# Performance work log

Measured on AMD Instinct MI355X. Metric: run time of the kernel, lower is better.

The kernel has to match this reference:

```python
import jax, jax.numpy as jnp
import numpy as np

NE, NPROC, E, D = 50000, 25000, 200000, 128
L, T = 3, 4  # layers, edge types: 0:e->e, 1:e->p, 2:p->p, 3:p->e


def setup_inputs() -> dict:
    key = jax.random.key(0)
    ks = jax.random.split(key, 17)
    s = 1.0 / np.sqrt(D)
    return {
        'x_elem': jax.random.normal(ks[0], (NE, D), jnp.float32),
        'x_proc': jax.random.normal(ks[1], (NPROC, D), jnp.float32),
        'W_src': jax.random.normal(ks[2], (L, T, D, D), jnp.float32) * s,
        'W_dst': jax.random.normal(ks[3], (L, T, D, D), jnp.float32) * s,
        'att_src': jax.random.normal(ks[4], (L, T, D), jnp.float32) * s,
        'att_dst': jax.random.normal(ks[5], (L, T, D), jnp.float32) * s,
        'bias': jax.random.normal(ks[6], (L, T, D), jnp.float32) * 0.01,
        'lin_W': jax.random.normal(ks[7], (D, 2), jnp.float32) * s,
        'lin_b': jnp.zeros((2,), jnp.float32),
        'ee_src': jax.random.randint(ks[8], (E,), 0, NE),
        'ee_dst': jax.random.randint(ks[9], (E,), 0, NE),
        'ep_src': jax.random.randint(ks[10], (E,), 0, NE),
        'ep_dst': jax.random.randint(ks[11], (E,), 0, NPROC),
        'pp_src': jax.random.randint(ks[12], (E,), 0, NPROC),
        'pp_dst': jax.random.randint(ks[13], (E,), 0, NPROC),
        'pe_src': jax.random.randint(ks[14], (E,), 0, NPROC),
        'pe_dst': jax.random.randint(ks[15], (E,), 0, NE),
    }


def _gat(x_s, x_d, src, dst, n_dst, Ws, Wd, a_s, a_d, b):
    # one GATConv (heads=1, negative_slope=0 -> relu, no self loops)
    hs = x_s @ Ws                       # [Ns, D]
    hd = x_d @ Wd                       # [Nd, D]
    es = hs @ a_s                       # [Ns]
    ed = hd @ a_d                       # [Nd]
    logit = jax.nn.relu(es[src] + ed[dst])              # [E]
    m = jax.ops.segment_max(logit, dst, num_segments=n_dst)
    m = jnp.where(jnp.isfinite(m), m, 0.0)              # empty segments
    w = jnp.exp(logit - m[dst])
    denom = jax.ops.segment_sum(w, dst, num_segments=n_dst)
    alpha = w / jnp.maximum(denom[dst], 1e-16)          # edge softmax per dst
    out = jax.ops.segment_sum(alpha[:, None] * hs[src], dst, num_segments=n_dst)
    return out + b


def reference(x_elem, x_proc, W_src, W_dst, att_src, att_dst, bias, lin_W, lin_b,
              ee_src, ee_dst, ep_src, ep_dst, pp_src, pp_dst, pe_src, pe_dst):
    xe, xp = x_elem, x_proc
    for l in range(L):
        ee = _gat(xe, xe, ee_src, ee_dst, NE, W_src[l, 0], W_dst[l, 0], att_src[l, 0], att_dst[l, 0], bias[l, 0])
        ep = _gat(xe, xp, ep_src, ep_dst, NPROC, W_src[l, 1], W_dst[l, 1], att_src[l, 1], att_dst[l, 1], bias[l, 1])
        pp = _gat(xp, xp, pp_src, pp_dst, NPROC, W_src[l, 2], W_dst[l, 2], att_src[l, 2], att_dst[l, 2], bias[l, 2])
        pe = _gat(xp, xe, pe_src, pe_dst, NE, W_src[l, 3], W_dst[l, 3], att_src[l, 3], att_dst[l, 3], bias[l, 3])
        xe = ee + pe   # to_hetero aggr='sum' per destination node type
        xp = ep + pp
    x = jnp.concatenate([xe, xp], axis=0) @ lin_W + lin_b  # G_aggr
    return x.mean(axis=0)  # [2]
```

## Files before the change

### kernel.cpp

```cpp
#include <hip/hip_runtime.h>

#define NE_N 50000
#define NP_N 25000
#define E_N 200000
#define DIM 128
#define LOG2E 1.4426950408889634f
#define NREP 1024

#define NCHK 32
#define CHK_E (E_N / NCHK)
#define TBL 16384

typedef __attribute__((ext_vector_type(8))) short short8;
typedef __attribute__((ext_vector_type(4))) float f32x4;
typedef __attribute__((ext_vector_type(2))) float f32x2;

static __device__ __forceinline__ ushort f2bf(float f) {
  unsigned x = __float_as_uint(f);
  return (ushort)((x + 0x7fffu + ((x >> 16) & 1u)) >> 16);
}
static __device__ __forceinline__ float bf2f(ushort u) {
  return __uint_as_float(((unsigned)u) << 16);
}

static __device__ __forceinline__ void gload_lds16(const void* g, void* l) {
  __builtin_amdgcn_global_load_lds(
      (const __attribute__((address_space(1))) void*)g,
      (__attribute__((address_space(3))) void*)l, 16, 0, 0);
}

#define HIST_BLKS (4 * NCHK)
#define HS_TOT (HIST_BLKS + 12 + 3)
__global__ __launch_bounds__(512) void hist_setup_k(
    const float* __restrict__ W_src, const float* __restrict__ W_dst,
    const float* __restrict__ att_dst, ushort* __restrict__ WbT,
    float* __restrict__ vec, const int* __restrict__ d0,
    const int* __restrict__ d1, const int* __restrict__ d2,
    const int* __restrict__ d3, unsigned char* __restrict__ h0,
    unsigned char* __restrict__ h1, unsigned char* __restrict__ h2,
    unsigned char* __restrict__ h3, ushort* __restrict__ rk0,
    ushort* __restrict__ rk1, ushort* __restrict__ rk2,
    ushort* __restrict__ rk3) {
  __shared__ int keys[TBL];
  __shared__ int cnts[TBL];
  const int blk = blockIdx.x;
  const int tid = threadIdx.x;
  if (blk < HIST_BLKS) {
    const int ty = blk >> 5, c = blk & (NCHK - 1);
    const int NN = (ty == 0 || ty == 3) ? NE_N : NP_N;
    const int* dst = ty == 0 ? d0 : ty == 1 ? d1 : ty == 2 ? d2 : d3;
    unsigned char* h = ty == 0 ? h0 : ty == 1 ? h1 : ty == 2 ? h2 : h3;
    ushort* rk = ty == 0 ? rk0 : ty == 1 ? rk1 : ty == 2 ? rk2 : rk3;
    for (int i = tid; i < TBL; i += 512) { keys[i] = -1; cnts[i] = 0; }
    __syncthreads();
    const int base = c * CHK_E;
    for (int i = tid; i < CHK_E; i += 512) {
      const int e = base + i;
      const int d = dst[e];
      unsigned hsh = ((unsigned)d * 2654435761u) >> 18;
      hsh &= (TBL - 1);
      int lr;
      while (true) {
        int prev = atomicCAS(&keys[hsh], -1, d);
        if (prev == -1 || prev == d) { lr = atomicAdd(&cnts[hsh], 1); break; }
        hsh = (hsh + 1) & (TBL - 1);
      }
      rk[e] = (ushort)lr;
    }
    __syncthreads();
    for (int i = tid; i < TBL; i += 512) {
      int k = keys[i];
      if (k >= 0) h[(size_t)c * NN + k] = (unsigned char)cnts[i];
    }
  } else if (blk < HIST_BLKS + 12) {
    const int w = blk - HIST_BLKS;
    const float* src = W_src + (size_t)w * DIM * DIM;
    ushort* dstw = WbT + (size_t)w * DIM * DIM;
    for (int i = tid; i < DIM * DIM; i += 512) {
      int k = i >> 7, n = i & 127;
      dstw[n * DIM + k] = f2bf(src[i]);
    }
  } else {
    const int b = blk - HIST_BLKS - 12;
    const int lt = b * 4 + (tid >> 7);
    const int i = tid & 127;
    const float* Wd = W_dst + (size_t)lt * DIM * DIM;
    const float* ad = att_dst + lt * DIM;
    float s = 0.f;
#pragma unroll 8
    for (int j = 0; j < DIM; j++) s += Wd[i * DIM + j] * ad[j];
    vec[lt * DIM + i] = s;
  }
}

__global__ __launch_bounds__(256) void scanA_k(
    unsigned char* __restrict__ h0, unsigned char* __restrict__ h1,
    unsigned char* __restrict__ h2, unsigned char* __restrict__ h3,
    int* __restrict__ c0, int* __restrict__ c1, int* __restrict__ c2,
    int* __restrict__ c3, int* __restrict__ part) {
  int ty = blockIdx.y;
  unsigned char* h = ty == 0 ? h0 : ty == 1 ? h1 : ty == 2 ? h2 : h3;
  int* cnt = ty == 0 ? c0 : ty == 1 ? c1 : ty == 2 ? c2 : c3;
  int n = (ty == 0 || ty == 3) ? NE_N : NP_N;
  int nblk = (n + 1023) >> 10;
  if ((int)blockIdx.x >= nblk) return;
  int base = blockIdx.x * 1024 + threadIdx.x * 4;
  int s = 0;
  if (base < n) {
    int run0 = 0, run1 = 0, run2 = 0, run3 = 0;
#pragma unroll
    for (int c = 0; c < NCHK; c++) {
      unsigned* hp = (unsigned*)(h + (size_t)c * n + base);
      unsigned v = *hp;
      *hp = (unsigned)(run0 & 255) | ((unsigned)(run1 & 255) << 8) |
            ((unsigned)(run2 & 255) << 16) | ((unsigned)(run3 & 255) << 24);
      run0 += (int)(v & 255u);
      run1 += (int)((v >> 8) & 255u);
      run2 += (int)((v >> 16) & 255u);
      run3 += (int)((v >> 24) & 255u);
    }
    cnt[base + 0] = run0; cnt[base + 1] = run1;
    cnt[base + 2] = run2; cnt[base + 3] = run3;
    s = run0 + run1 + run2 + run3;
  }
  int lane = threadIdx.x & 63, wid = threadIdx.x >> 6;
#pragma unroll
  for (int off = 32; off > 0; off >>= 1) s += __shfl_xor(s, off, 64);
  __shared__ int ws4[4];
  if (lane == 0) ws4[wid] = s;
  __syncthreads();
  if (threadIdx.x == 0)
    part[ty * 64 + blockIdx.x] = ws4[0] + ws4[1] + ws4[2] + ws4[3];
}

__global__ __launch_bounds__(256) void scanBC_k(
    const int* __restrict__ c0, const int* __restrict__ c1,
    const int* __restrict__ c2, const int* __restrict__ c3,
    int* __restrict__ r0, int* __restrict__ r1, int* __restrict__ r2,
    int* __restrict__ r3, const int* __restrict__ part) {
  int ty = blockIdx.y;
  int bx = blockIdx.x;
  const int* cnt = ty == 0 ? c0 : ty == 1 ? c1 : ty == 2 ? c2 : c3;
  int* rp = ty == 0 ? r0 : ty == 1 ? r1 : ty == 2 ? r2 : r3;
  int n = (ty == 0 || ty == 3) ? NE_N : NP_N;
  int nblk = (n + 1023) >> 10;
  if (bx >= nblk) return;

  __shared__ int s_excl;
  if (threadIdx.x < 64) {
    int pl = threadIdx.x;
    int v = (pl < nblk) ? part[ty * 64 + pl] : 0;
    int sc = v;
#pragma unroll
    for (int off = 1; off < 64; off <<= 1) {
      int t = __shfl_up(sc, off, 64);
      if (pl >= off) sc += t;
    }
    if (pl == bx) s_excl = sc - v;
  }
  if (bx == 0 && threadIdx.x == 0) rp[n] = E_N;
  __syncthreads();

  int base = bx * 1024 + threadIdx.x * 4;
  int v[4];
#pragma unroll
  for (int j = 0; j < 4; j++) v[j] = (base + j < n) ? cnt[base + j] : 0;
  int s = v[0] + v[1] + v[2] + v[3];
  int lane = threadIdx.x & 63, wid = threadIdx.x >> 6;
  int sc = s;
#pragma unroll
  for (int off = 1; off < 64; off <<= 1) {
    int t = __shfl_up(sc, off, 64);
    if (lane >= off) sc += t;
  }
  __shared__ int ws4[4];
  if (lane == 63) ws4[wid] = sc;
  __syncthreads();
  int wbase = 0;
  for (int w = 0; w < wid; w++) wbase += ws4[w];
  int p = s_excl + wbase + sc - s;
#pragma unroll
  for (int j = 0; j < 4; j++) {
    if (base + j < n) rp[base + j] = p;
    p += v[j];
  }
}

#define EBLK ((NE_N + 255) / 256)
#define PBLK ((NP_N + 255) / 256)
#define GEMM_BLK (EBLK + PBLK)
#define FILL_PER_CHK 13
#define FILL_BLKS (4 * NCHK * FILL_PER_CHK)
#define HG2_TOT (GEMM_BLK + FILL_BLKS)

template <bool FP32>
static __device__ __forceinline__ void x_prefetch(
    const void* xb, int rowA, int quad, float4* xraw, short8* xvv) {
  if (FP32) {
    const float* xf32 = (const float*)xb + (size_t)rowA * DIM + quad * 8;
#pragma unroll
    for (int k0 = 0; k0 < 4; k0++) {
      xraw[2 * k0] = *(const float4*)(xf32 + k0 * 32);
      xraw[2 * k0 + 1] = *(const float4*)(xf32 + k0 * 32 + 4);
    }
  } else {
    const ushort* xb16 = (const ushort*)xb + (size_t)rowA * DIM + quad * 8;
#pragma unroll
    for (int k0 = 0; k0 < 4; k0++)
      xvv[k0] = *(const short8*)(xb16 + k0 * 32);
  }
}

template <bool FP32>
static __device__ __forceinline__ void strip_body(
    int row0, int N, int m, int quad, int lane, const short8* wlds,
    const float* dv0, const float* dv1, const float* a0, const float* a1,
    unsigned char* hs0, unsigned char* hs1, float* es0, float* es1,
    float* edA, float* edB, float4* xraw, short8* xvv) {
  float edp0 = 0.f, edp1 = 0.f;
#pragma unroll
  for (int k0 = 0; k0 < 4; k0++) {
    float xf[8];
    if (FP32) {
      float4 f0 = xraw[2 * k0], f1 = xraw[2 * k0 + 1];
      xf[0] = f0.x; xf[1] = f0.y; xf[2] = f0.z; xf[3] = f0.w;
      xf[4] = f1.x; xf[5] = f1.y; xf[6] = f1.z; xf[7] = f1.w;
      short8 xv;
#pragma unroll
      for (int j = 0; j < 8; j++) xv[j] = (short)f2bf(xf[j]);
      xvv[k0] = xv;
    } else {
#pragma unroll
      for (int j = 0; j < 8; j++) xf[j] = bf2f((ushort)xvv[k0][j]);
    }
    int off = k0 * 32 + quad * 8;
    float4 vA0 = *(const float4*)&dv0[off];
    float4 vA1 = *(const float4*)&dv0[off + 4];
    float4 vB0 = *(const float4*)&dv1[off];
    float4 vB1 = *(const float4*)&dv1[off + 4];
    edp0 += xf[0] * vA0.x + xf[1] * vA0.y + xf[2] * vA0.z + xf[3] * vA0.w +
            xf[4] * vA1.x + xf[5] * vA1.y + xf[6] * vA1.z + xf[7] * vA1.w;
    edp1 += xf[0] * vB0.x + xf[1] * vB0.y + xf[2] * vB0.z + xf[3] * vB0.w +
            xf[4] * vB1.x + xf[5] * vB1.y + xf[6] * vB1.z + xf[7] * vB1.w;
  }

  f32x4 acc0[8], acc1[8];
#pragma unroll
  for (int f = 0; f < 8; f++) {
    acc0[f] = (f32x4){0.f, 0.f, 0.f, 0.f};
    acc1[f] = (f32x4){0.f, 0.f, 0.f, 0.f};
  }
#pragma unroll
  for (int k0 = 0; k0 < 4; k0++) {
    const short8 xv = xvv[k0];
#pragma unroll
    for (int f = 0; f < 8; f++) {
      acc0[f] = __builtin_amdgcn_mfma_f32_16x16x32_bf16(
          wlds[(k0 * 8 + f) * 64 + lane], xv, acc0[f], 0, 0, 0);
      acc1[f] = __builtin_amdgcn_mfma_f32_16x16x32_bf16(
          wlds[2048 + (k0 * 8 + f) * 64 + lane], xv, acc1[f], 0, 0, 0);
    }
  }

  const int row = row0 + m;
  edp0 += __shfl_xor(edp0, 16, 64);
  edp0 += __shfl_xor(edp0, 32, 64);
  edp1 += __shfl_xor(edp1, 16, 64);
  edp1 += __shfl_xor(edp1, 32, 64);
  if (quad == 0 && row < N) {
    edA[row] = edp0 * LOG2E;
    edB[row] = edp1 * LOG2E;
  }

#pragma unroll
  for (int set = 0; set < 2; set++) {
    f32x4* acc = set ? acc1 : acc0;
    const float* as = set ? a1 : a0;
    float* es = set ? es1 : es0;
    unsigned char* hs = set ? hs1 : hs0;

    float esum = 0.f;
#pragma unroll
    for (int f = 0; f < 8; f++) {
      float4 av = *(const float4*)&as[f * 16 + quad * 4];
      esum += acc[f][0] * av.x + acc[f][1] * av.y + acc[f][2] * av.z +
              acc[f][3] * av.w;
    }
    esum += __shfl_xor(esum, 16, 64);
    esum += __shfl_xor(esum, 32, 64);
    if (quad == 0 && row < N) es[row] = esum * LOG2E;

    if (row < N) {
#pragma unroll
      for (int f = 0; f < 8; f++) {
        int w = __builtin_amdgcn_cvt_pk_fp8_f32(acc[f][0], acc[f][1], 0, false);
        w = __builtin_amdgcn_cvt_pk_fp8_f32(acc[f][2], acc[f][3], w, true);
        *(unsigned*)&hs[(size_t)row * DIM + f * 16 + quad * 4] = (unsigned)w;
      }
    }
  }
}

template <bool FP32>
static __device__ __forceinline__ void gemm_body(
    int blk, const void* __restrict__ xev, const void* __restrict__ xpv,
    const ushort* __restrict__ WbT, const float* __restrict__ att,
    const float* __restrict__ vec, int l, unsigned char* __restrict__ hsE0,
    unsigned char* __restrict__ hsE1, unsigned char* __restrict__ hsP3,
    unsigned char* __restrict__ hsP2, float* __restrict__ esE0,
    float* __restrict__ esE1, float* __restrict__ esP3,
    float* __restrict__ esP2, float* __restrict__ edEA,
    float* __restrict__ edEB, float* __restrict__ edPA,
    float* __restrict__ edPB) {
  const void* xb;
  const ushort *W0T, *W1T;
  const float *a0, *a1, *dv0, *dv1;
  unsigned char *hs0, *hs1;
  float *es0, *es1, *edA, *edB;
  int N, rbase;
  if (blk < EBLK) {
    xb = xev; N = NE_N; rbase = blk * 256;
    W0T = WbT + (size_t)(l * 4 + 0) * DIM * DIM;
    W1T = WbT + (size_t)(l * 4 + 1) * DIM * DIM;
    a0 = att + (l * 4 + 0) * DIM; a1 = att + (l * 4 + 1) * DIM;
    dv0 = vec + (l * 4 + 0) * DIM; dv1 = vec + (l * 4 + 3) * DIM;
    hs0 = hsE0; hs1 = hsE1; es0 = esE0; es1 = esE1;
    edA = edEA; edB = edEB;
  } else {
    blk -= EBLK; xb = xpv; N = NP_N; rbase = blk * 256;
    W0T = WbT + (size_t)(l * 4 + 3) * DIM * DIM;
    W1T = WbT + (size_t)(l * 4 + 2) * DIM * DIM;
    a0 = att + (l * 4 + 3) * DIM; a1 = att + (l * 4 + 2) * DIM;
    dv0 = vec + (l * 4 + 1) * DIM; dv1 = vec + (l * 4 + 2) * DIM;
    hs0 = hsP3; hs1 = hsP2; es0 = esP3; es1 = esP2;
    edA = edPA; edB = edPB;
  }

  const int wave = threadIdx.x >> 6;
  const int lane = threadIdx.x & 63;
  const int m = lane & 15, quad = lane >> 4;
  const int row0A = rbase + wave * 16;
  const int row0B = rbase + 128 + wave * 16;
  int rowLA = row0A + m; if (rowLA >= N) rowLA = N - 1;
  int rowLB = row0B + m; if (rowLB >= N) rowLB = N - 1;

  float4 xrawA[8]; short8 xvvA[4];
  x_prefetch<FP32>(xb, rowLA, quad, xrawA, xvvA);

  __shared__ short8 wlds[4096];
  {
    const int i15 = lane & 15, i4 = lane >> 4;
#pragma unroll
    for (int r = 0; r < 8; r++) {
      const int g = r * 8 + wave;
      const int set = g >> 5, k0 = (g >> 3) & 3, f = g & 7;
      const ushort* WT = set ? W1T : W0T;
      gload_lds16(WT + (size_t)(f * 16 + i15) * DIM + k0 * 32 + i4 * 8,
                  &wlds[g * 64]);
    }
  }
  __syncthreads();

  float4 xrawB[8]; short8 xvvB[4];
  if (!FP32) x_prefetch<FP32>(xb, rowLB, quad, xrawB, xvvB);

  if (row0A < N)
    strip_body<FP32>(row0A, N, m, quad, lane, wlds, dv0, dv1, a0, a1,
                     hs0, hs1, es0, es1, edA, edB, xrawA, xvvA);
  if (FP32) x_prefetch<FP32>(xb, rowLB, quad, xrawB, xvvB);
  if (row0B < N)
    strip_body<FP32>(row0B, N, m, quad, lane, wlds, dv0, dv1, a0, a1,
                     hs0, hs1, es0, es1, edA, edB, xrawB, xvvB);
}

__global__ __launch_bounds__(512, 4) void gemm_k(
    const ushort* __restrict__ xe, const ushort* __restrict__ xp,
    const ushort* __restrict__ WbT, const float* __restrict__ att,
    const float* __restrict__ vec, int l, unsigned char* __restrict__ hsE0,
    unsigned char* __restrict__ hsE1, unsigned char* __restrict__ hsP3,
    unsigned char* __restrict__ hsP2, float* __restrict__ esE0,
    float* __restrict__ esE1, float* __restrict__ esP3,
    float* __restrict__ esP2, float* __restrict__ edEA,
    float* __restrict__ edEB, float* __restrict__ edPA,
    float* __restrict__ edPB) {
  gemm_body<false>(blockIdx.x, xe, xp, WbT, att, vec, l, hsE0, hsE1, hsP3,
                   hsP2, esE0, esE1, esP3, esP2, edEA, edEB, edPA, edPB);
}

__global__ __launch_bounds__(512, 4) void fill_gemm0_k(
    const float* __restrict__ xe, const float* __restrict__ xp,
    const ushort* __restrict__ WbT, const float* __restrict__ att,
    const float* __restrict__ vec, unsigned char* __restrict__ hsE0,
    unsigned char* __restrict__ hsE1, unsigned char* __restrict__ hsP3,
    unsigned char* __restrict__ hsP2, float* __restrict__ esE0,
    float* __restrict__ esE1, float* __restrict__ esP3,
    float* __restrict__ esP2, float* __restrict__ edEA,
    float* __restrict__ edEB, float* __restrict__ edPA,
    float* __restrict__ edPB, const int* __restrict__ s0,
    const int* __restrict__ s1, const int* __restrict__ s2,
    const int* __restrict__ s3, const int* __restrict__ d0,
    const int* __restrict__ d1, const int* __restrict__ d2,
    const int* __restrict__ d3, const ushort* __restrict__ rk0,
    const ushort* __restrict__ rk1, const ushort* __restrict__ rk2,
    const ushort* __restrict__ rk3, const int* __restrict__ r0,
    const int* __restrict__ r1, const int* __restrict__ r2,
    const int* __restrict__ r3, const unsigned char* __restrict__ h0,
    const unsigned char* __restrict__ h1, const unsigned char* __restrict__ h2,
    const unsigned char* __restrict__ h3, ushort* __restrict__ o0,
    ushort* __restrict__ o1, ushort* __restrict__ o2,
    ushort* __restrict__ o3) {
  const int blk = blockIdx.x;
  if (blk < GEMM_BLK) {
    gemm_body<true>(blk, xe, xp, WbT, att, vec, 0, hsE0, hsE1, hsP3, hsP2,
                    esE0, esE1, esP3, esP2, edEA, edEB, edPA, edPB);
  } else {
    const int fb = blk - GEMM_BLK;
    const int x = fb & 7, q = fb >> 3;
    const int g = ((q & 15) << 3) | x;
    const int j = q >> 4;
    const int i = j * 512 + threadIdx.x;
    if (i >= CHK_E) return;
    const int ty = g >> 5, c = g & 31;
    const int e = c * CHK_E + i;
    const int NN = (ty == 0 || ty == 3) ? NE_N : NP_N;
    const int* src = ty == 0 ? s0 : ty == 1 ? s1 : ty == 2 ? s2 : s3;
    const int* dst = ty == 0 ? d0 : ty == 1 ? d1 : ty == 2 ? d2 : d3;
    const ushort* rk = ty == 0 ? rk0 : ty == 1 ? rk1 : ty == 2 ? rk2 : rk3;
    const int* rp = ty == 0 ? r0 : ty == 1 ? r1 : ty == 2 ? r2 : r3;
    const unsigned char* ho = ty == 0 ? h0 : ty == 1 ? h1 : ty == 2 ? h2 : h3;
    ushort* out = ty == 0 ? o0 : ty == 1 ? o1 : ty == 2 ? o2 : o3;
    const int dd = dst[e];
    out[rp[dd] + (int)ho[(size_t)c * NN + dd] + (int)rk[e]] =
        (ushort)src[e];
  }
}

__global__ __launch_bounds__(256) void gat_gather_all(
    const int* __restrict__ rp0, const ushort* __restrict__ ss0,
    const int* __restrict__ rp1, const ushort* __restrict__ ss1,
    const int* __restrict__ rp2, const ushort* __restrict__ ss2,
    const int* __restrict__ rp3, const ushort* __restrict__ ss3,
    const float* __restrict__ esE0, const unsigned char* __restrict__ hsE0,
    const float* __restrict__ esE1, const unsigned char* __restrict__ hsE1,
    const float* __restrict__ esP3, const unsigned char* __restrict__ hsP3,
    const float* __restrict__ esP2, const unsigned char* __restrict__ hsP2,
    const float* __restrict__ edEA, const float* __restrict__ edEB,
    const float* __restrict__ edPA, const float* __restrict__ edPB,
    const float* __restrict__ bias, int l, ushort* __restrict__ outxe,
    ushort* __restrict__ outxp, int to_csum, float* __restrict__ csum_rep) {
  __shared__ float2 trx[4][8][64];
  const int wid = (blockIdx.x * 256 + threadIdx.x) >> 6;
  const int lane = threadIdx.x & 63;
  const int wv = threadIdx.x >> 6;
  const int slot = lane >> 3, sub = lane & 7;
  const int half = slot >> 2;
  const int hslot = slot & 3;
  const bool active = wid < NE_N + NP_N;

  float v0 = 0.f, v1 = 0.f;
  const float *b0 = bias, *b1 = bias;
  ushort* outb = outxe;
  int node = 0;

  if (active) {
    const int *rpA, *rpB;
    const ushort *ssA, *ssB;
    const float *esA, *esB;
    const unsigned char *hsA, *hsB;
    const float *edA, *edB;
    if (wid < NE_N) {
      node = wid;
      rpA = rp0; ssA = ss0; esA = esE0; hsA = hsE0;
      rpB = rp3; ssB = ss3; esB = esP3; hsB = hsP3;
      edA = edEA; edB = edEB;
      b0 = bias + (l * 4 + 0) * DIM; b1 = bias + (l * 4 + 3) * DIM;
      outb = outxe;
    } else {
      node = wid - NE_N;
      rpA = rp1; ssA = ss1; esA = esE1; hsA = hsE1;
      rpB = rp2; ssB = ss2; esB = esP2; hsB = hsP2;
      edA = edPA; edB = edPB;
      b0 = bias + (l * 4 + 1) * DIM; b1 = bias + (l * 4 + 2) * DIM;
      outb = outxp;
    }

    const int* rp = half ? rpB : rpA;
    const ushort* ss = half ? ssB : ssA;
    const float* es = half ? esB : esA;
    const unsigned char* hs = half ? hsB : hsA;
    const float edv = half ? edB[node] : edA[node];
    const int beg = rp[node], end = rp[node + 1];

    f32x2 acc2[8];
#pragma unroll
    for (int j = 0; j < 8; j++) acc2[j] = (f32x2){0.f, 0.f};
    float sw = 0.f;

    for (int e = beg + hslot; e < end; e += 4) {
      int s = ss[e];
      float w = exp2f(fmaxf(es[s] + edv, 0.f));
      sw += w;
      f32x2 w2 = {w, w};
      uint4 h = *(const uint4*)&hs[(size_t)s * DIM + sub * 16];
      acc2[0] += w2 * __builtin_amdgcn_cvt_pk_f32_fp8((int)h.x, false);
      acc2[1] += w2 * __builtin_amdgcn_cvt_pk_f32_fp8((int)h.x, true);
      acc2[2] += w2 * __builtin_amdgcn_cvt_pk_f32_fp8((int)h.y, false);
      acc2[3] += w2 * __builtin_amdgcn_cvt_pk_f32_fp8((int)h.y, true);
      acc2[4] += w2 * __builtin_amdgcn_cvt_pk_f32_fp8((int)h.z, false);
      acc2[5] += w2 * __builtin_amdgcn_cvt_pk_f32_fp8((int)h.z, true);
      acc2[6] += w2 * __builtin_amdgcn_cvt_pk_f32_fp8((int)h.w, false);
      acc2[7] += w2 * __builtin_amdgcn_cvt_pk_f32_fp8((int)h.w, true);
    }

    sw += __shfl_xor(sw, 8, 64);
    sw += __shfl_xor(sw, 16, 64);
    const float inv = 1.f / fmaxf(sw, 1e-16f);

#pragma unroll
    for (int j = 0; j < 8; j++)
      trx[wv][slot][(sub * 8 + j) ^ slot] =
          make_float2(acc2[j].x * inv, acc2[j].y * inv);
    float2 vv = trx[wv][0][(sub * 8 + slot) ^ 0];
#pragma unroll
    for (int s2 = 1; s2 < 8; s2++) {
      float2 t = trx[wv][s2][(sub * 8 + slot) ^ s2];
      vv.x += t.x;
      vv.y += t.y;
    }
    v0 = vv.x;
    v1 = vv.y;
  }

  const int d = sub * 16 + slot * 2;
  if (to_csum) {
    __shared__ float lsum[4][DIM];
    lsum[wv][d] = v0;
    lsum[wv][d + 1] = v1;
    __syncthreads();
    if (threadIdx.x < DIM) {
      float s = lsum[0][threadIdx.x] + lsum[1][threadIdx.x] +
                lsum[2][threadIdx.x] + lsum[3][threadIdx.x];
      float* rep = csum_rep + (size_t)(blockIdx.x & (NREP - 1)) * DIM;
      unsafeAtomicAdd(&rep[threadIdx.x], s);
    }
  } else if (active) {
    float2 bb0 = *(const float2*)&b0[d];
    float2 bb1 = *(const float2*)&b1[d];
    ushort2 o;
    o.x = f2bf(v0 + bb0.x + bb1.x);
    o.y = f2bf(v1 + bb0.y + bb1.y);
    *(ushort2*)&outb[(size_t)node * DIM + d] = o;
  }
}

__global__ __launch_bounds__(512) void final_proj(
    const float* __restrict__ csum_rep, const float* __restrict__ bias,
    const float* __restrict__ lin_W, const float* __restrict__ lin_b,
    float* __restrict__ out) {
  __shared__ float parts[4][DIM];
  __shared__ float col[DIM];
  const int k = threadIdx.x & 127;
  const int pt = threadIdx.x >> 7;
  float s = 0.f;
#pragma unroll 8
  for (int r = pt * (NREP / 4); r < (pt + 1) * (NREP / 4); r++)
    s += csum_rep[(size_t)r * DIM + k];
  parts[pt][k] = s;
  __syncthreads();
  if (threadIdx.x < DIM) {
    const float* bE0 = bias + (2 * 4 + 0) * DIM;
    const float* bE1 = bias + (2 * 4 + 3) * DIM;
    const float* bP0 = bias + (2 * 4 + 1) * DIM;
    const float* bP1 = bias + (2 * 4 + 2) * DIM;
    col[k] = parts[0][k] + parts[1][k] + parts[2][k] + parts[3][k] +
             (float)NE_N * (bE0[k] + bE1[k]) +
             (float)NP_N * (bP0[k] + bP1[k]);
  }
  __syncthreads();
  if (threadIdx.x < 2) {
    float acc = 0.f;
#pragma unroll 8
    for (int j = 0; j < DIM; j++) acc += col[j] * lin_W[j * 2 + threadIdx.x];
    out[threadIdx.x] = acc / (float)(NE_N + NP_N) + lin_b[threadIdx.x];
  }
}

extern "C" void kernel_launch(void* const* d_in, const int* in_sizes, int n_in,
                              void* d_out, int out_size, void* d_ws,
                              size_t ws_size, hipStream_t stream) {
  const float* x_elem  = (const float*)d_in[0];
  const float* x_proc  = (const float*)d_in[1];
  const float* W_src   = (const float*)d_in[2];
  const float* W_dst   = (const float*)d_in[3];
  const float* att_src = (const float*)d_in[4];
  const float* att_dst = (const float*)d_in[5];
  const float* bias    = (const float*)d_in[6];
  const float* lin_W   = (const float*)d_in[7];
  const float* lin_b   = (const float*)d_in[8];
  const int* esrc[4] = {(const int*)d_in[9],  (const int*)d_in[11],
                        (const int*)d_in[13], (const int*)d_in[15]};
  const int* edst[4] = {(const int*)d_in[10], (const int*)d_in[12],
                        (const int*)d_in[14], (const int*)d_in[16]};

  char* p = (char*)d_ws;
  ushort* xe_bf[2]; ushort* xp_bf[2];
  xe_bf[0] = (ushort*)p; p += (size_t)NE_N * DIM * 2;
  xe_bf[1] = (ushort*)p; p += (size_t)NE_N * DIM * 2;
  xp_bf[0] = (ushort*)p; p += (size_t)NP_N * DIM * 2;
  xp_bf[1] = (ushort*)p; p += (size_t)NP_N * DIM * 2;
  unsigned char* hsE0 = (unsigned char*)p; p += (size_t)NE_N * DIM;
  unsigned char* hsE1 = (unsigned char*)p; p += (size_t)NE_N * DIM;
  unsigned char* hsP3 = (unsigned char*)p; p += (size_t)NP_N * DIM;
  unsigned char* hsP2 = (unsigned char*)p; p += (size_t)NP_N * DIM;
  ushort* WbT = (ushort*)p; p += (size_t)12 * DIM * DIM * 2;
  float* esE0 = (float*)p; p += (size_t)NE_N * 4;
  float* esE1 = (float*)p; p += (size_t)NE_N * 4;
  float* esP3 = (float*)p; p += (size_t)NP_N * 4;
  float* esP2 = (float*)p; p += (size_t)NP_N * 4;
  float* edEA = (float*)p; p += (size_t)NE_N * 4;
  float* edEB = (float*)p; p += (size_t)NE_N * 4;
  float* edPA = (float*)p; p += (size_t)NP_N * 4;
  float* edPB = (float*)p; p += (size_t)NP_N * 4;
  float* vec = (float*)p; p += 12 * DIM * 4;
  int* parti = (int*)p; p += 4 * 64 * 4;
  float* csum_rep = (float*)p; p += (size_t)NREP * DIM * 4;
  unsigned char* hh[4];
  hh[0] = (unsigned char*)p; p += (size_t)NE_N * NCHK;
  hh[1] = (unsigned char*)p; p += (size_t)NP_N * NCHK;
  hh[2] = (unsigned char*)p; p += (size_t)NP_N * NCHK;
  hh[3] = (unsigned char*)p; p += (size_t)NE_N * NCHK;
  int* cnt[4];
  for (int t = 0; t < 4; t++) { cnt[t] = (int*)p; p += (NE_N + 4) * 4; }
  int* rp[4];
  for (int t = 0; t < 4; t++) { rp[t] = (int*)p; p += (NE_N + 4) * 4; }
  ushort* ssrc[4];
  for (int t = 0; t < 4; t++) { ssrc[t] = (ushort*)p; p += (size_t)E_N * 2; }
  ushort* rank[4];
  for (int t = 0; t < 4; t++) { rank[t] = (ushort*)p; p += (size_t)E_N * 2; }

  hipMemsetAsync(csum_rep, 0,
                 (size_t)NREP * DIM * 4 +
                     (size_t)(2 * NE_N + 2 * NP_N) * NCHK,
                 stream);

  hist_setup_k<<<HS_TOT, 512, 0, stream>>>(
      W_src, W_dst, att_dst, WbT, vec, edst[0], edst[1], edst[2], edst[3],
      hh[0], hh[1], hh[2], hh[3], rank[0], rank[1], rank[2], rank[3]);

  scanA_k<<<dim3(49, 4), 256, 0, stream>>>(hh[0], hh[1], hh[2], hh[3],
                                           cnt[0], cnt[1], cnt[2], cnt[3],
                                           parti);
  scanBC_k<<<dim3(49, 4), 256, 0, stream>>>(cnt[0], cnt[1], cnt[2], cnt[3],
                                            rp[0], rp[1], rp[2], rp[3], parti);

  fill_gemm0_k<<<HG2_TOT, 512, 0, stream>>>(
      x_elem, x_proc, WbT, att_src, vec, hsE0, hsE1, hsP3, hsP2, esE0, esE1,
      esP3, esP2, edEA, edEB, edPA, edPB, esrc[0], esrc[1], esrc[2], esrc[3],
      edst[0], edst[1], edst[2], edst[3], rank[0], rank[1], rank[2], rank[3],
      rp[0], rp[1], rp[2], rp[3], hh[0], hh[1], hh[2], hh[3],
      ssrc[0], ssrc[1], ssrc[2], ssrc[3]);

  int c = 0;
  for (int l = 0; l < 3; l++) {
    if (l > 0) {
      gemm_k<<<GEMM_BLK, 512, 0, stream>>>(
          xe_bf[c], xp_bf[c], WbT, att_src, vec, l, hsE0, hsE1, hsP3, hsP2,
          esE0, esE1, esP3, esP2, edEA, edEB, edPA, edPB);
    }
    int to_csum = (l == 2) ? 1 : 0;
    gat_gather_all<<<(NE_N + NP_N) / 4, 256, 0, stream>>>(
        rp[0], ssrc[0], rp[1], ssrc[1], rp[2], ssrc[2], rp[3], ssrc[3], esE0,
        hsE0, esE1, hsE1, esP3, hsP3, esP2, hsP2, edEA, edEB, edPA, edPB,
        bias, l, xe_bf[1 - c], xp_bf[1 - c], to_csum, csum_rep);
    c = 1 - c;
  }

  final_proj<<<1, 512, 0, stream>>>(csum_rep, bias, lin_W, lin_b,
                                    (float*)d_out);
}
```

Baseline: 382.7 us.

## Split fused gemm0/fill kernel and unroll gather loop by two edges

```diff
diff --git a/kernel.cpp b/kernel.cpp
--- a/kernel.cpp
+++ b/kernel.cpp
@@ -191,7 +191,6 @@
 #define GEMM_BLK (EBLK + PBLK)
 #define FILL_PER_CHK 13
 #define FILL_BLKS (4 * NCHK * FILL_PER_CHK)
-#define HG2_TOT (GEMM_BLK + FILL_BLKS)
 
 template <bool FP32>
 static __device__ __forceinline__ void x_prefetch(
@@ -387,7 +386,7 @@
                    hsP2, esE0, esE1, esP3, esP2, edEA, edEB, edPA, edPB);
 }
 
-__global__ __launch_bounds__(512, 4) void fill_gemm0_k(
+__global__ __launch_bounds__(512, 4) void gemm0_k(
     const float* __restrict__ xe, const float* __restrict__ xp,
     const ushort* __restrict__ WbT, const float* __restrict__ att,
     const float* __restrict__ vec, unsigned char* __restrict__ hsE0,
@@ -396,43 +395,41 @@
     float* __restrict__ esE1, float* __restrict__ esP3,
     float* __restrict__ esP2, float* __restrict__ edEA,
     float* __restrict__ edEB, float* __restrict__ edPA,
-    float* __restrict__ edPB, const int* __restrict__ s0,
-    const int* __restrict__ s1, const int* __restrict__ s2,
-    const int* __restrict__ s3, const int* __restrict__ d0,
-    const int* __restrict__ d1, const int* __restrict__ d2,
-    const int* __restrict__ d3, const ushort* __restrict__ rk0,
-    const ushort* __restrict__ rk1, const ushort* __restrict__ rk2,
-    const ushort* __restrict__ rk3, const int* __restrict__ r0,
-    const int* __restrict__ r1, const int* __restrict__ r2,
-    const int* __restrict__ r3, const unsigned char* __restrict__ h0,
-    const unsigned char* __restrict__ h1, const unsigned char* __restrict__ h2,
-    const unsigned char* __restrict__ h3, ushort* __restrict__ o0,
-    ushort* __restrict__ o1, ushort* __restrict__ o2,
-    ushort* __restrict__ o3) {
-  const int blk = blockIdx.x;
-  if (blk < GEMM_BLK) {
-    gemm_body<true>(blk, xe, xp, WbT, att, vec, 0, hsE0, hsE1, hsP3, hsP2,
-                    esE0, esE1, esP3, esP2, edEA, edEB, edPA, edPB);
-  } else {
-    const int fb = blk - GEMM_BLK;
-    const int x = fb & 7, q = fb >> 3;
-    const int g = ((q & 15) << 3) | x;
-    const int j = q >> 4;
-    const int i = j * 512 + threadIdx.x;
-    if (i >= CHK_E) return;
-    const int ty = g >> 5, c = g & 31;
-    const int e = c * CHK_E + i;
-    const int NN = (ty == 0 || ty == 3) ? NE_N : NP_N;
-    const int* src = ty == 0 ? s0 : ty == 1 ? s1 : ty == 2 ? s2 : s3;
-    const int* dst = ty == 0 ? d0 : ty == 1 ? d1 : ty == 2 ? d2 : d3;
-    const ushort* rk = ty == 0 ? rk0 : ty == 1 ? rk1 : ty == 2 ? rk2 : rk3;
-    const int* rp = ty == 0 ? r0 : ty == 1 ? r1 : ty == 2 ? r2 : r3;
-    const unsigned char* ho = ty == 0 ? h0 : ty == 1 ? h1 : ty == 2 ? h2 : h3;
-    ushort* out = ty == 0 ? o0 : ty == 1 ? o1 : ty == 2 ? o2 : o3;
-    const int dd = dst[e];
-    out[rp[dd] + (int)ho[(size_t)c * NN + dd] + (int)rk[e]] =
-        (ushort)src[e];
-  }
+    float* __restrict__ edPB) {
+  gemm_body<true>(blockIdx.x, xe, xp, WbT, att, vec, 0, hsE0, hsE1, hsP3,
+                  hsP2, esE0, esE1, esP3, esP2, edEA, edEB, edPA, edPB);
+}
+
+__global__ __launch_bounds__(512) void fill_k(
+    const int* __restrict__ s0, const int* __restrict__ s1,
+    const int* __restrict__ s2, const int* __restrict__ s3,
+    const int* __restrict__ d0, const int* __restrict__ d1,
+    const int* __restrict__ d2, const int* __restrict__ d3,
+    const ushort* __restrict__ rk0, const ushort* __restrict__ rk1,
+    const ushort* __restrict__ rk2, const ushort* __restrict__ rk3,
+    const int* __restrict__ r0, const int* __restrict__ r1,
+    const int* __restrict__ r2, const int* __restrict__ r3,
+    const unsigned char* __restrict__ h0, const unsigned char* __restrict__ h1,
+    const unsigned char* __restrict__ h2, const unsigned char* __restrict__ h3,
+    ushort* __restrict__ o0, ushort* __restrict__ o1,
+    ushort* __restrict__ o2, ushort* __restrict__ o3) {
+  const int fb = blockIdx.x;
+  const int x = fb & 7, q = fb >> 3;
+  const int g = ((q & 15) << 3) | x;
+  const int j = q >> 4;
+  const int i = j * 512 + threadIdx.x;
+  if (i >= CHK_E) return;
+  const int ty = g >> 5, c = g & 31;
+  const int e = c * CHK_E + i;
+  const int NN = (ty == 0 || ty == 3) ? NE_N : NP_N;
+  const int* src = ty == 0 ? s0 : ty == 1 ? s1 : ty == 2 ? s2 : s3;
+  const int* dst = ty == 0 ? d0 : ty == 1 ? d1 : ty == 2 ? d2 : d3;
+  const ushort* rk = ty == 0 ? rk0 : ty == 1 ? rk1 : ty == 2 ? rk2 : rk3;
+  const int* rp = ty == 0 ? r0 : ty == 1 ? r1 : ty == 2 ? r2 : r3;
+  const unsigned char* ho = ty == 0 ? h0 : ty == 1 ? h1 : ty == 2 ? h2 : h3;
+  ushort* out = ty == 0 ? o0 : ty == 1 ? o1 : ty == 2 ? o2 : o3;
+  const int dd = dst[e];
+  out[rp[dd] + (int)ho[(size_t)c * NN + dd] + (int)rk[e]] = (ushort)src[e];
 }
 
 __global__ __launch_bounds__(256) void gat_gather_all(
@@ -496,12 +493,45 @@
     for (int j = 0; j < 8; j++) acc2[j] = (f32x2){0.f, 0.f};
     float sw = 0.f;
 
-    for (int e = beg + hslot; e < end; e += 4) {
+    int e = beg + hslot;
+    for (; e + 4 < end; e += 8) {
+      int sA = ss[e];
+      int sB = ss[e + 4];
+      float wA = exp2f(fmaxf(es[sA] + edv, 0.f));
+      float wB = exp2f(fmaxf(es[sB] + edv, 0.f));
+      uint4 hA = *(const uint4*)&hs[(size_t)sA * DIM + sub * 16];
+      uint4 hB = *(const uint4*)&hs[(size_t)sB * DIM + sub * 16];
+      sw += wA;
+      {
+        f32x2 w2 = {wA, wA};
+        acc2[0] += w2 * __builtin_amdgcn_cvt_pk_f32_fp8((int)hA.x, false);
+        acc2[1] += w2 * __builtin_amdgcn_cvt_pk_f32_fp8((int)hA.x, true);
+        acc2[2] += w2 * __builtin_amdgcn_cvt_pk_f32_fp8((int)hA.y, false);
+        acc2[3] += w2 * __builtin_amdgcn_cvt_pk_f32_fp8((int)hA.y, true);
+        acc2[4] += w2 * __builtin_amdgcn_cvt_pk_f32_fp8((int)hA.z, false);
+        acc2[5] += w2 * __builtin_amdgcn_cvt_pk_f32_fp8((int)hA.z, true);
+        acc2[6] += w2 * __builtin_amdgcn_cvt_pk_f32_fp8((int)hA.w, false);
+        acc2[7] += w2 * __builtin_amdgcn_cvt_pk_f32_fp8((int)hA.w, true);
+      }
+      sw += wB;
+      {
+        f32x2 w2 = {wB, wB};
+        acc2[0] += w2 * __builtin_amdgcn_cvt_pk_f32_fp8((int)hB.x, false);
+        acc2[1] += w2 * __builtin_amdgcn_cvt_pk_f32_fp8((int)hB.x, true);
+        acc2[2] += w2 * __builtin_amdgcn_cvt_pk_f32_fp8((int)hB.y, false);
+        acc2[3] += w2 * __builtin_amdgcn_cvt_pk_f32_fp8((int)hB.y, true);
+        acc2[4] += w2 * __builtin_amdgcn_cvt_pk_f32_fp8((int)hB.z, false);
+        acc2[5] += w2 * __builtin_amdgcn_cvt_pk_f32_fp8((int)hB.z, true);
+        acc2[6] += w2 * __builtin_amdgcn_cvt_pk_f32_fp8((int)hB.w, false);
+        acc2[7] += w2 * __builtin_amdgcn_cvt_pk_f32_fp8((int)hB.w, true);
+      }
+    }
+    if (e < end) {
       int s = ss[e];
       float w = exp2f(fmaxf(es[s] + edv, 0.f));
+      uint4 h = *(const uint4*)&hs[(size_t)s * DIM + sub * 16];
       sw += w;
       f32x2 w2 = {w, w};
-      uint4 h = *(const uint4*)&hs[(size_t)s * DIM + sub * 16];
       acc2[0] += w2 * __builtin_amdgcn_cvt_pk_f32_fp8((int)h.x, false);
       acc2[1] += w2 * __builtin_amdgcn_cvt_pk_f32_fp8((int)h.x, true);
       acc2[2] += w2 * __builtin_amdgcn_cvt_pk_f32_fp8((int)h.y, false);
@@ -653,12 +683,13 @@
   scanBC_k<<<dim3(49, 4), 256, 0, stream>>>(cnt[0], cnt[1], cnt[2], cnt[3],
                                             rp[0], rp[1], rp[2], rp[3], parti);
 
-  fill_gemm0_k<<<HG2_TOT, 512, 0, stream>>>(
+  gemm0_k<<<GEMM_BLK, 512, 0, stream>>>(
       x_elem, x_proc, WbT, att_src, vec, hsE0, hsE1, hsP3, hsP2, esE0, esE1,
-      esP3, esP2, edEA, edEB, edPA, edPB, esrc[0], esrc[1], esrc[2], esrc[3],
-      edst[0], edst[1], edst[2], edst[3], rank[0], rank[1], rank[2], rank[3],
-      rp[0], rp[1], rp[2], rp[3], hh[0], hh[1], hh[2], hh[3],
-      ssrc[0], ssrc[1], ssrc[2], ssrc[3]);
+      esP3, esP2, edEA, edEB, edPA, edPB);
+  fill_k<<<FILL_BLKS, 512, 0, stream>>>(
+      esrc[0], esrc[1], esrc[2], esrc[3], edst[0], edst[1], edst[2], edst[3],
+      rank[0], rank[1], rank[2], rank[3], rp[0], rp[1], rp[2], rp[3],
+      hh[0], hh[1], hh[2], hh[3], ssrc[0], ssrc[1], ssrc[2], ssrc[3]);
 
   int c = 0;
   for (int l = 0; l < 3; l++) {
```

New measurement: 426.6 us. 1.11x slower.
